# Optimization experiments

Hardware: AMD Instinct MI355X
Metric: run time of the kernel (lower is better)

Reference implementation:

```python
import jax, jax.numpy as jnp
import numpy as np


def _matrix_sqrt(x, iter_n=3):
    # Newton-Schulz iteration for batched matrix square root. x: [B, d, d]
    norm = jnp.linalg.norm(x, axis=(1, 2), keepdims=True)
    Y = x / (norm + 1e-8)
    d = x.shape[1]
    I = jnp.broadcast_to(jnp.eye(d, dtype=x.dtype), x.shape)
    Z = I
    for _ in range(iter_n):
        T = 0.5 * (3.0 * I - Z @ Y)
        Y = Y @ T
        Z = T @ Z
    return Y * jnp.sqrt(norm + 1e-8)


def _l2norm(x, eps=1e-12):
    n = jnp.linalg.norm(x, axis=-1, keepdims=True)
    return x / jnp.maximum(n, eps)


def _tukey(x, beta=0.5):
    return jnp.sign(x) * jnp.power(jnp.abs(x) + 1e-8, beta)


def _components(feat, cov_reducer, w_bls, b_bls):
    # feat: [Bx, N, D] patch tokens for one layer
    gap = feat.mean(axis=1)                                   # [Bx, D]
    x = feat @ cov_reducer                                    # [Bx, N, P]
    x = x - x.mean(axis=1, keepdims=True)
    denom = max(1, feat.shape[1] - 1)
    cov = jnp.einsum('bnp,bnq->bpq', x, x) / denom            # [Bx, P, P]
    P = cov.shape[-1]
    cov = cov + 1e-5 * jnp.eye(P, dtype=cov.dtype)
    cs = _matrix_sqrt(cov)
    iu = np.triu_indices(P)
    cov_flat = cs[:, iu[0], iu[1]]                            # [Bx, P*(P+1)/2]
    bls = jnp.tanh(feat @ w_bls + b_bls).mean(axis=1)         # [Bx, W]
    return gap, cov_flat, bls


def _fuse(gap, cov, bls, n_views):
    # gap/cov/bls: [L, Bx, F_l]; concat layers, pool views, tukey + l2 + weight
    def proc(t, w):
        Bx = t.shape[1]
        t = jnp.moveaxis(t, 0, 1).reshape(Bx, -1)             # cat over layers
        t = t.reshape(-1, n_views, t.shape[-1]).mean(axis=1)  # TTA view pooling
        return _l2norm(_tukey(t)) * w
    return jnp.concatenate([proc(gap, 1.0), proc(cov, 0.8), proc(bls, 0.1)], axis=-1)


def _forward(feats_sup, feats_qry, cov_reducer, w_bls, b_bls, y_sup, B, n_views, num_classes):
    comp = jax.vmap(_components, in_axes=(0, None, None, None))
    gs, cs, bs = comp(feats_sup, cov_reducer, w_bls, b_bls)
    gq, cq, bq = comp(feats_qry, cov_reducer, w_bls, b_bls)
    z_sup = _fuse(gs, cs, bs, n_views)
    z_qry = _fuse(gq, cq, bq, n_views)
    z_sup = z_sup.reshape(B, -1, z_sup.shape[-1])             # [B, n_sup, d]
    z_qry = z_qry.reshape(B, -1, z_qry.shape[-1])             # [B, n_qry, d]
    mu_sup = z_sup.mean(axis=1, keepdims=True)
    std_sup = jnp.std(z_sup, axis=1, keepdims=True, ddof=1) + 1e-8
    mu_qry = z_qry.mean(axis=1, keepdims=True)
    std_qry = jnp.std(z_qry, axis=1, keepdims=True, ddof=1) + 1e-8
    z_qry = (z_qry - mu_qry) / std_qry * std_sup + mu_sup
    z_sup = _l2norm(z_sup - mu_sup)
    z_qry = _l2norm(z_qry - mu_sup)
    Y = jax.nn.one_hot(y_sup, num_classes, dtype=z_sup.dtype)
    d_feat = z_sup.shape[-1]
    lam = 0.1 * (d_feat / 500.0)
    n_sup = z_sup.shape[1]
    K = jnp.einsum('bnd,bmd->bnm', z_sup, z_sup)
    alpha = jnp.linalg.solve(K + lam * jnp.eye(n_sup, dtype=K.dtype), Y)
    sim = jnp.einsum('bqd,bnd->bqn', z_qry, z_sup)
    return (sim @ alpha) * 20.0


def setup_inputs() -> dict:
    key = jax.random.key(0)
    ks = jax.random.split(key, 5)
    L, N, D, P = 2, 196, 768, 64
    B, n_sup, n_qry, n_views = 2, 25, 50, 5
    feats_sup = jax.random.normal(ks[0], (L, B * n_sup * n_views, N, D), jnp.float32)
    feats_qry = jax.random.normal(ks[1], (L, B * n_qry * n_views, N, D), jnp.float32)
    y_sup = jax.random.randint(ks[2], (B, n_sup), 0, 5)
    cov_reducer = jax.random.normal(ks[3], (D, P), jnp.float32) / jnp.sqrt(jnp.float32(D))
    w_bls = jax.random.normal(ks[4], (D, D), jnp.float32) / jnp.sqrt(jnp.float32(D))
    b_bls = jnp.zeros((D,), jnp.float32)
    return {"feats_sup": feats_sup, "feats_qry": feats_qry, "cov_reducer": cov_reducer,
            "w_bls": w_bls, "b_bls": b_bls, "y_sup": y_sup, "B": B, "n_views": n_views,
            "num_classes": 5}


def reference(feats_sup, feats_qry, cov_reducer, w_bls, b_bls, y_sup, B, n_views, num_classes):
    return _forward(feats_sup, feats_qry, cov_reducer, w_bls, b_bls, y_sup, B, n_views, num_classes)
```

## Files before the change

### kernel.cpp

```cpp
#include <hip/hip_runtime.h>
#include <stdint.h>
#include <math.h>

typedef __bf16 bf16x8_t __attribute__((ext_vector_type(8)));
typedef float  f32x4_t  __attribute__((ext_vector_type(4)));

constexpr int NTOK = 196;
constexpr int DF   = 768;
constexpr int PD   = 64;
constexpr int NSAMP = 1500;
constexpr int SUPS  = 500;
constexpr int PFLAT = 2080;
constexpr int FTOT  = 7232;
constexpr size_t FEAT_ELEMS = (size_t)NTOK * DF;

constexpr size_t SZ_FEATB = (size_t)NSAMP * FEAT_ELEMS * 2;
constexpr size_t OFF_FEATB = 0;
constexpr size_t OFF_WT    = OFF_FEATB + SZ_FEATB;
constexpr size_t SZ_WT     = (size_t)DF * DF * 2;
constexpr size_t OFF_RTH   = OFF_WT + SZ_WT;
constexpr size_t SZ_RT     = (size_t)PD * DF * 2;
constexpr size_t OFF_RTL   = OFF_RTH + SZ_RT;
constexpr size_t OFF_GAP   = OFF_RTL + SZ_RT;
constexpr size_t SZ_GAP    = (size_t)NSAMP * DF * 4;
constexpr size_t OFF_BLS   = OFF_GAP + SZ_GAP;
constexpr size_t OFF_COVF  = OFF_BLS + SZ_GAP;
constexpr size_t SZ_COVF   = (size_t)NSAMP * PFLAT * 4;
constexpr size_t OFF_Z     = OFF_COVF + SZ_COVF;
constexpr size_t SZ_Z      = (size_t)150 * FTOT * 4;
constexpr size_t OFF_ZN    = OFF_Z + SZ_Z;
constexpr size_t OFF_STATS = OFF_ZN + SZ_Z;
constexpr size_t SZ_STATS  = (size_t)4 * 2 * FTOT * 4;
constexpr size_t OFF_KM    = OFF_STATS + SZ_STATS;
constexpr size_t OFF_SIM   = OFF_KM + 5120;

__device__ __forceinline__ unsigned short f2bf(float f) {
    unsigned int u = __float_as_uint(f);
    u += 0x7fffu + ((u >> 16) & 1u);
    return (unsigned short)(u >> 16);
}
__device__ __forceinline__ float bf2f(unsigned short h) {
    return __uint_as_float(((unsigned int)h) << 16);
}
__device__ __forceinline__ void async_copy16(void* lds, const void* g) {
    __builtin_amdgcn_global_load_lds(
        (const __attribute__((address_space(1))) unsigned int*)g,
        (__attribute__((address_space(3))) unsigned int*)lds, 16, 0, 0);
}
__device__ __forceinline__ f32x4_t mfma16(bf16x8_t a, bf16x8_t b, f32x4_t c) {
    return __builtin_amdgcn_mfma_f32_16x16x32_bf16(a, b, c, 0, 0, 0);
}
__device__ __forceinline__ float tukeyf(float x) {
    float s = (x > 0.f) ? 1.f : ((x < 0.f) ? -1.f : 0.f);
    return s * sqrtf(fabsf(x) + 1e-8f);
}
__device__ __forceinline__ float blockReduceSum(float v, float* scratch) {
    for (int m = 1; m < 64; m <<= 1) v += __shfl_xor(v, m);
    int w = threadIdx.x >> 6, lane = threadIdx.x & 63;
    if (lane == 0) scratch[w] = v;
    __syncthreads();
    float r = scratch[0] + scratch[1] + scratch[2] + scratch[3];
    __syncthreads();
    return r;
}

__global__ __launch_bounds__(256) void k_prep(const float* __restrict__ W,
                                              const float* __restrict__ red,
                                              unsigned short* __restrict__ Wt,
                                              unsigned short* __restrict__ rTh,
                                              unsigned short* __restrict__ rTl) {
    int tid = blockIdx.x * 256 + threadIdx.x;
    int stride = gridDim.x * 256;
    for (int idx = tid; idx < DF * DF; idx += stride) {
        int d = idx / DF, k = idx % DF;
        Wt[idx] = f2bf(W[k * DF + d]);
    }
    for (int idx = tid; idx < PD * DF; idx += stride) {
        int p = idx / DF, k = idx % DF;
        float v = red[k * PD + p];
        unsigned short h = f2bf(v);
        rTh[idx] = h;
        rTl[idx] = f2bf(v - bf2f(h));
    }
}

__global__ __launch_bounds__(256) void k_sample(const float* __restrict__ fsup,
                                                const float* __restrict__ fqry,
                                                const unsigned short* __restrict__ rTh,
                                                const unsigned short* __restrict__ rTl,
                                                unsigned short* __restrict__ featB,
                                                float* __restrict__ gapB,
                                                float* __restrict__ covF) {
    __shared__ __align__(16) char smem[67840];
    unsigned short* Ahi = (unsigned short*)smem;
    unsigned short* Alo = Ahi + 8192;
    unsigned short* Bhi = Alo + 8192;
    unsigned short* Blo = Bhi + 2048;
    float* xT    = (float*)smem;
    float* covB  = (float*)(smem + 50432);
    float* gscr  = (float*)(smem + 50432 + 16640);
    float* means = (float*)(smem + 50432 + 16640 + 512);

    int sid = blockIdx.x;
    const float* fbase = (sid < SUPS) ? (fsup + (size_t)sid * FEAT_ELEMS)
                                      : (fqry + (size_t)(sid - SUPS) * FEAT_ELEMS);
    unsigned short* fB = featB + (size_t)sid * FEAT_ELEMS;

    int t = threadIdx.x;
    int w = t >> 6, lane = t & 63;
    int kgroup = t & 7, rbase = t >> 3;

    f32x4_t acc[4][4];
    f32x4_t z4 = {0.f, 0.f, 0.f, 0.f};
    #pragma unroll
    for (int i = 0; i < 4; ++i)
        #pragma unroll
        for (int j = 0; j < 4; ++j) acc[i][j] = z4;

    for (int k0 = 0; k0 < DF; k0 += 32) {
        float gx = 0.f, gy = 0.f, gz = 0.f, gw = 0.f;
        #pragma unroll
        for (int it = 0; it < 8; ++it) {
            int row = rbase + 32 * it;
            int n = row < NTOK ? row : (NTOK - 1);
            float4 v = *(const float4*)(fbase + (size_t)n * DF + k0 + kgroup * 4);
            unsigned short h0 = f2bf(v.x), h1 = f2bf(v.y), h2 = f2bf(v.z), h3 = f2bf(v.w);
            ushort4 hv; hv.x = h0; hv.y = h1; hv.z = h2; hv.w = h3;
            ushort4 lv;
            lv.x = f2bf(v.x - bf2f(h0)); lv.y = f2bf(v.y - bf2f(h1));
            lv.z = f2bf(v.z - bf2f(h2)); lv.w = f2bf(v.w - bf2f(h3));
            *(ushort4*)(Ahi + row * 32 + kgroup * 4) = hv;
            *(ushort4*)(Alo + row * 32 + kgroup * 4) = lv;
            if (row < NTOK) {
                gx += v.x; gy += v.y; gz += v.z; gw += v.w;
                *(ushort4*)(fB + (size_t)row * DF + k0 + kgroup * 4) = hv;
            }
        }
        gx += __shfl_xor(gx, 8);  gy += __shfl_xor(gy, 8);  gz += __shfl_xor(gz, 8);  gw += __shfl_xor(gw, 8);
        gx += __shfl_xor(gx, 16); gy += __shfl_xor(gy, 16); gz += __shfl_xor(gz, 16); gw += __shfl_xor(gw, 16);
        gx += __shfl_xor(gx, 32); gy += __shfl_xor(gy, 32); gz += __shfl_xor(gz, 32); gw += __shfl_xor(gw, 32);
        if (lane < 8) {
            gscr[w * 32 + lane * 4 + 0] = gx; gscr[w * 32 + lane * 4 + 1] = gy;
            gscr[w * 32 + lane * 4 + 2] = gz; gscr[w * 32 + lane * 4 + 3] = gw;
        }
        {
            int p = t >> 2, kq = t & 3;
            *(bf16x8_t*)(Bhi + p * 32 + kq * 8) = *(const bf16x8_t*)(rTh + (size_t)p * DF + k0 + kq * 8);
            *(bf16x8_t*)(Blo + p * 32 + kq * 8) = *(const bf16x8_t*)(rTl + (size_t)p * DF + k0 + kq * 8);
        }
        __syncthreads();
        if (t < 32) {
            float s = gscr[t] + gscr[32 + t] + gscr[64 + t] + gscr[96 + t];
            gapB[(size_t)sid * DF + k0 + t] = s * (1.f / 196.f);
        }
        bf16x8_t ah[4], al[4], bh[4], bl[4];
        int krow = (lane >> 4) * 8;
        #pragma unroll
        for (int i = 0; i < 4; ++i) {
            int aoff = (w * 64 + i * 16 + (lane & 15)) * 32 + krow;
            ah[i] = *(const bf16x8_t*)&Ahi[aoff];
            al[i] = *(const bf16x8_t*)&Alo[aoff];
        }
        #pragma unroll
        for (int j = 0; j < 4; ++j) {
            int boff = (j * 16 + (lane & 15)) * 32 + krow;
            bh[j] = *(const bf16x8_t*)&Bhi[boff];
            bl[j] = *(const bf16x8_t*)&Blo[boff];
        }
        #pragma unroll
        for (int i = 0; i < 4; ++i)
            #pragma unroll
            for (int j = 0; j < 4; ++j) {
                acc[i][j] = mfma16(ah[i], bh[j], acc[i][j]);
                acc[i][j] = mfma16(ah[i], bl[j], acc[i][j]);
                acc[i][j] = mfma16(al[i], bh[j], acc[i][j]);
            }
        __syncthreads();
    }

    int quad = lane >> 4, col = lane & 15;
    #pragma unroll
    for (int i = 0; i < 4; ++i)
        #pragma unroll
        for (int j = 0; j < 4; ++j)
            #pragma unroll
            for (int r = 0; r < 4; ++r) {
                int rowN = w * 64 + i * 16 + quad * 4 + r;
                if (rowN < NTOK) xT[(j * 16 + col) * 197 + rowN] = acc[i][j][r];
            }
    __syncthreads();
    if (t < 64) {
        float s = 0.f;
        for (int n = 0; n < NTOK; ++n) s += xT[t * 197 + n];
        means[t] = s * (1.f / 196.f);
    }
    __syncthreads();
    {
        int p = t & 63;
        for (int n = t >> 6; n < NTOK; n += 4) xT[p * 197 + n] -= means[p];
    }
    __syncthreads();
    int tp = t >> 4, tq = t & 15;
    {
        float cc[4][4] = {{0.f}};
        for (int k = 0; k < NTOK; ++k) {
            float a_[4], b_[4];
            #pragma unroll
            for (int i = 0; i < 4; ++i) a_[i] = xT[(4 * tp + i) * 197 + k];
            #pragma unroll
            for (int j = 0; j < 4; ++j) b_[j] = xT[(4 * tq + j) * 197 + k];
            #pragma unroll
            for (int i = 0; i < 4; ++i)
                #pragma unroll
                for (int j = 0; j < 4; ++j) cc[i][j] += a_[i] * b_[j];
        }
        float ssq = 0.f;
        #pragma unroll
        for (int i = 0; i < 4; ++i)
            #pragma unroll
            for (int j = 0; j < 4; ++j) {
                int gi = 4 * tp + i, gj = 4 * tq + j;
                float cv = cc[i][j] * (1.f / 195.f);
                if (gi == gj) cv += 1e-5f;
                covB[gi * 65 + gj] = cv;
                ssq += cv * cv;
            }
        float tot = blockReduceSum(ssq, gscr);
        float norm = sqrtf(tot);
        float rn = 1.f / (norm + 1e-8f);
        float scs = sqrtf(norm + 1e-8f);
        float* Yp = xT;
        float* Zp = xT + 4160;
        float* Up = xT + 8320;
        float* Tp = covB;
        for (int e = 0; e < 16; ++e) {
            int idx = t + 256 * e;
            int i = idx >> 6, j = idx & 63;
            Yp[i * 65 + j] = covB[i * 65 + j] * rn;
            Zp[i * 65 + j] = (i == j) ? 1.f : 0.f;
        }
        __syncthreads();

        for (int itn = 0; itn < 3; ++itn) {
            {
                float dd[4][4] = {{0.f}};
                for (int k = 0; k < 64; ++k) {
                    float a_[4], b_[4];
                    #pragma unroll
                    for (int i = 0; i < 4; ++i) a_[i] = Zp[(4 * tp + i) * 65 + k];
                    #pragma unroll
                    for (int j = 0; j < 4; ++j) b_[j] = Yp[k * 65 + 4 * tq + j];
                    #pragma unroll
                    for (int i = 0; i < 4; ++i)
                        #pragma unroll
                        for (int j = 0; j < 4; ++j) dd[i][j] += a_[i] * b_[j];
                }
                #pragma unroll
                for (int i = 0; i < 4; ++i)
                    #pragma unroll
                    for (int j = 0; j < 4; ++j) {
                        int gi = 4 * tp + i, gj = 4 * tq + j;
                        Tp[gi * 65 + gj] = 0.5f * (((gi == gj) ? 3.f : 0.f) - dd[i][j]);
                    }
            }
            __syncthreads();
            {
                float dd[4][4] = {{0.f}};
                for (int k = 0; k < 64; ++k) {
                    float a_[4], b_[4];
                    #pragma unroll
                    for (int i = 0; i < 4; ++i) a_[i] = Yp[(4 * tp + i) * 65 + k];
                    #pragma unroll
                    for (int j = 0; j < 4; ++j) b_[j] = Tp[k * 65 + 4 * tq + j];
                    #pragma unroll
                    for (int i = 0; i < 4; ++i)
                        #pragma unroll
                        for (int j = 0; j < 4; ++j) dd[i][j] += a_[i] * b_[j];
                }
                #pragma unroll
                for (int i = 0; i < 4; ++i)
                    #pragma unroll
                    for (int j = 0; j < 4; ++j) Up[(4 * tp + i) * 65 + 4 * tq + j] = dd[i][j];
            }
            __syncthreads();
            {
                float dd[4][4] = {{0.f}};
                for (int k = 0; k < 64; ++k) {
                    float a_[4], b_[4];
                    #pragma unroll
                    for (int i = 0; i < 4; ++i) a_[i] = Tp[(4 * tp + i) * 65 + k];
                    #pragma unroll
                    for (int j = 0; j < 4; ++j) b_[j] = Zp[k * 65 + 4 * tq + j];
                    #pragma unroll
                    for (int i = 0; i < 4; ++i)
                        #pragma unroll
                        for (int j = 0; j < 4; ++j) dd[i][j] += a_[i] * b_[j];
                }
                #pragma unroll
                for (int i = 0; i < 4; ++i)
                    #pragma unroll
                    for (int j = 0; j < 4; ++j) Yp[(4 * tp + i) * 65 + 4 * tq + j] = dd[i][j];
            }
            __syncthreads();
            float* ny = Up; float* nz = Yp; float* nu = Zp;
            Yp = ny; Zp = nz; Up = nu;
        }
        for (int idx = t; idx < PFLAT; idx += 256) {
            float disc = 129.f * 129.f - 8.f * (float)idx;
            int i = (int)((129.f - sqrtf(disc)) * 0.5f);
            if (i > 63) i = 63; if (i < 0) i = 0;
            while (i < 63 && ((i + 1) * 64 - ((i + 1) * i) / 2) <= idx) ++i;
            while (i > 0 && (i * 64 - (i * (i - 1)) / 2) > idx) --i;
            int S = i * 64 - (i * (i - 1)) / 2;
            int j = idx - S + i;
            covF[(size_t)sid * PFLAT + idx] = Yp[i * 65 + j] * scs;
        }
    }
}

__global__ __launch_bounds__(256) void k_bls(const unsigned short* __restrict__ featB,
                                             const unsigned short* __restrict__ Wt,
                                             const float* __restrict__ b_bls,
                                             float* __restrict__ blsB) {
    __shared__ unsigned short Al[128 * 32];
    __shared__ unsigned short Bl[128 * 32];
    __shared__ float colsum[128];

    int blk = blockIdx.x;
    int sid = blk / 6, dt = blk % 6;
    int d0 = dt * 128;
    size_t sidElems = (size_t)sid * FEAT_ELEMS;

    int t = threadIdx.x;
    int w = t >> 6, lane = t & 63;
    int wm = w >> 1, wn = w & 1;
    if (t < 128) colsum[t] = 0.f;

    for (int mt = 0; mt < 2; ++mt) {
        int m0 = mt * 128;
        f32x4_t acc[4][4];
        f32x4_t z4 = {0.f, 0.f, 0.f, 0.f};
        #pragma unroll
        for (int i = 0; i < 4; ++i)
            #pragma unroll
            for (int j = 0; j < 4; ++j) acc[i][j] = z4;

        for (int k0 = 0; k0 < DF; k0 += 32) {
            #pragma unroll
            for (int jj = 0; jj < 2; ++jj) {
                int j = 2 * w + jj;
                int row = j * 16 + (lane >> 2);
                int chunk = lane & 3;
                int gr = m0 + row; gr = gr > 195 ? 195 : gr;
                async_copy16((char*)Al + j * 1024 + lane * 16,
                             featB + sidElems + (size_t)gr * DF + k0 + chunk * 8);
                async_copy16((char*)Bl + j * 1024 + lane * 16,
                             Wt + (size_t)(d0 + row) * DF + k0 + chunk * 8);
            }
            __syncthreads();

            bf16x8_t af[4], bfr[4];
            int krow = (lane >> 4) * 8;
            #pragma unroll
            for (int i = 0; i < 4; ++i)
                af[i] = *(const bf16x8_t*)&Al[(wm * 64 + i * 16 + (lane & 15)) * 32 + krow];
            #pragma unroll
            for (int j = 0; j < 4; ++j)
                bfr[j] = *(const bf16x8_t*)&Bl[(wn * 64 + j * 16 + (lane & 15)) * 32 + krow];
            #pragma unroll
            for (int i = 0; i < 4; ++i)
                #pragma unroll
                for (int j = 0; j < 4; ++j)
                    acc[i][j] = mfma16(af[i], bfr[j], acc[i][j]);
            __syncthreads();
        }
        int quad = lane >> 4, col = lane & 15;
        #pragma unroll
        for (int j = 0; j < 4; ++j) {
            int dl = wn * 64 + j * 16 + col;
            float bb = b_bls[d0 + dl];
            float psum = 0.f;
            #pragma unroll
            for (int i = 0; i < 4; ++i)
                #pragma unroll
                for (int r = 0; r < 4; ++r) {
                    int rowN = m0 + wm * 64 + i * 16 + quad * 4 + r;
                    if (rowN < NTOK) psum += tanhf(acc[i][j][r] + bb);
                }
            psum += __shfl_xor(psum, 16);
            psum += __shfl_xor(psum, 32);
            if (quad == 0) atomicAdd(&colsum[dl], psum);
        }
    }
    __syncthreads();
    if (t < 128) blsB[(size_t)sid * DF + d0 + t] = colsum[t] * (1.f / 196.f);
}

__global__ __launch_bounds__(256) void k_fuse(const float* __restrict__ gapB,
                                              const float* __restrict__ covF,
                                              const float* __restrict__ blsB,
                                              float* __restrict__ z) {
    __shared__ float zrow[FTOT];
    __shared__ float scr[8];
    int r = blockIdx.x, t = threadIdx.x;
    bool isSup = r < 50;
    int g = isSup ? r : r - 50;

    float ss0 = 0.f, ss1 = 0.f, ss2 = 0.f;
    for (int f = t; f < DF; f += 256) {
        for (int l = 0; l < 2; ++l) {
            float s = 0.f;
            for (int v = 0; v < 5; ++v) {
                int sid = isSup ? (l * 250 + g * 5 + v) : (500 + l * 500 + g * 5 + v);
                s += gapB[(size_t)sid * DF + f];
            }
            float tk = tukeyf(s * 0.2f);
            zrow[l * DF + f] = tk;
            ss0 += tk * tk;
        }
    }
    for (int f = t; f < PFLAT; f += 256) {
        for (int l = 0; l < 2; ++l) {
            float s = 0.f;
            for (int v = 0; v < 5; ++v) {
                int sid = isSup ? (l * 250 + g * 5 + v) : (500 + l * 500 + g * 5 + v);
                s += covF[(size_t)sid * PFLAT + f];
            }
            float tk = tukeyf(s * 0.2f);
            zrow[1536 + l * PFLAT + f] = tk;
            ss1 += tk * tk;
        }
    }
    for (int f = t; f < DF; f += 256) {
        for (int l = 0; l < 2; ++l) {
            float s = 0.f;
            for (int v = 0; v < 5; ++v) {
                int sid = isSup ? (l * 250 + g * 5 + v) : (500 + l * 500 + g * 5 + v);
                s += blsB[(size_t)sid * DF + f];
            }
            float tk = tukeyf(s * 0.2f);
            zrow[5696 + l * DF + f] = tk;
            ss2 += tk * tk;
        }
    }
    __syncthreads();
    float n0 = blockReduceSum(ss0, scr);
    float n1 = blockReduceSum(ss1, scr);
    float n2 = blockReduceSum(ss2, scr);
    float s0 = 1.0f / fmaxf(sqrtf(n0), 1e-12f);
    float s1 = 0.8f / fmaxf(sqrtf(n1), 1e-12f);
    float s2 = 0.1f / fmaxf(sqrtf(n2), 1e-12f);
    for (int f = t; f < FTOT; f += 256) {
        float sc = (f < 1536) ? s0 : ((f < 5696) ? s1 : s2);
        z[(size_t)r * FTOT + f] = zrow[f] * sc;
    }
}

__global__ __launch_bounds__(256) void k_stats(const float* __restrict__ z,
                                               float* __restrict__ stats) {
    int f = blockIdx.x * 256 + threadIdx.x;
    int b = blockIdx.y;
    if (f >= FTOT) return;
    float mu = 0.f;
    for (int i = 0; i < 25; ++i) mu += z[(size_t)(b * 25 + i) * FTOT + f];
    mu *= (1.f / 25.f);
    float var = 0.f;
    for (int i = 0; i < 25; ++i) { float d = z[(size_t)(b * 25 + i) * FTOT + f] - mu; var += d * d; }
    float sds = sqrtf(var * (1.f / 24.f)) + 1e-8f;
    float muq = 0.f;
    for (int q = 0; q < 50; ++q) muq += z[(size_t)(50 + b * 50 + q) * FTOT + f];
    muq *= (1.f / 50.f);
    float varq = 0.f;
    for (int q = 0; q < 50; ++q) { float d = z[(size_t)(50 + b * 50 + q) * FTOT + f] - muq; varq += d * d; }
    float sdq = sqrtf(varq * (1.f / 49.f)) + 1e-8f;
    stats[(0 * 2 + b) * FTOT + f] = mu;
    stats[(1 * 2 + b) * FTOT + f] = sds;
    stats[(2 * 2 + b) * FTOT + f] = muq;
    stats[(3 * 2 + b) * FTOT + f] = sdq;
}

__global__ __launch_bounds__(256) void k_norm2(const float* __restrict__ z,
                                               const float* __restrict__ stats,
                                               float* __restrict__ zn) {
    __shared__ float scr[8];
    int r = blockIdx.x, t = threadIdx.x;
    bool isSup = r < 50;
    int b = isSup ? (r / 25) : ((r - 50) / 50);
    const float* mu_s = stats + (size_t)(0 * 2 + b) * FTOT;
    const float* sd_s = stats + (size_t)(1 * 2 + b) * FTOT;
    const float* mu_q = stats + (size_t)(2 * 2 + b) * FTOT;
    const float* sd_q = stats + (size_t)(3 * 2 + b) * FTOT;
    float ssq = 0.f;
    for (int f = t; f < FTOT; f += 256) {
        float v;
        float zv = z[(size_t)r * FTOT + f];
        if (isSup) v = zv - mu_s[f];
        else {
            float q = (zv - mu_q[f]) / sd_q[f] * sd_s[f] + mu_s[f];
            v = q - mu_s[f];
        }
        zn[(size_t)r * FTOT + f] = v;
        ssq += v * v;
    }
    float tot = blockReduceSum(ssq, scr);
    float sc = 1.f / fmaxf(sqrtf(tot), 1e-12f);
    for (int f = t; f < FTOT; f += 256) zn[(size_t)r * FTOT + f] *= sc;
}

__global__ __launch_bounds__(256) void k_gram(const float* __restrict__ zn,
                                              float* __restrict__ Km,
                                              float* __restrict__ simB) {
    __shared__ float scr[8];
    int r = blockIdx.x, t = threadIdx.x;
    bool isSup = r < 50;
    int b = isSup ? (r / 25) : ((r - 50) / 50);
    const float* a = zn + (size_t)r * FTOT;
    for (int j = 0; j < 25; ++j) {
        const float* bj = zn + (size_t)(b * 25 + j) * FTOT;
        float p = 0.f;
        for (int f = t; f < FTOT; f += 256) p += a[f] * bj[f];
        float tot = blockReduceSum(p, scr);
        if (t == 0) {
            if (isSup) Km[b * 625 + (r - b * 25) * 25 + j] = tot;
            else       simB[b * 1250 + (r - 50 - b * 50) * 25 + j] = tot;
        }
    }
}

__global__ __launch_bounds__(256) void k_solve(const float* __restrict__ Km,
                                               const float* __restrict__ simB,
                                               const int* __restrict__ y_sup,
                                               float* __restrict__ out) {
    __shared__ float A[25][31];
    __shared__ float alpha[25][5];
    int b = blockIdx.x, t = threadIdx.x;
    const float lam = 0.1f * (7232.0f / 500.0f);
    for (int idx = t; idx < 625; idx += 256) {
        int i = idx / 25, j = idx % 25;
        A[i][j] = Km[b * 625 + idx] + ((i == j) ? lam : 0.f);
    }
    for (int idx = t; idx < 125; idx += 256) {
        int i = idx / 5, c = idx % 5;
        A[i][25 + c] = (y_sup[b * 25 + i] == c) ? 1.f : 0.f;
    }
    __syncthreads();
    for (int k = 0; k < 25; ++k) {
        if (t > k && t < 25) {
            float f = A[t][k] / A[k][k];
            for (int c = k; c < 30; ++c) A[t][c] -= f * A[k][c];
        }
        __syncthreads();
    }
    for (int k = 24; k >= 0; --k) {
        if (t < 5) {
            float s = A[k][25 + t];
            for (int j = k + 1; j < 25; ++j) s -= A[k][j] * alpha[j][t];
            alpha[k][t] = s / A[k][k];
        }
        __syncthreads();
    }
    for (int idx = t; idx < 250; idx += 256) {
        int q = idx / 5, c = idx % 5;
        float s = 0.f;
        for (int n = 0; n < 25; ++n) s += simB[b * 1250 + q * 25 + n] * alpha[n][c];
        out[(b * 50 + q) * 5 + c] = 20.f * s;
    }
}

extern "C" void kernel_launch(void* const* d_in, const int* in_sizes, int n_in,
                              void* d_out, int out_size, void* d_ws, size_t ws_size,
                              hipStream_t stream) {
    const float* fsup  = (const float*)d_in[0];
    const float* fqry  = (const float*)d_in[1];
    const float* red   = (const float*)d_in[2];
    const float* Wb    = (const float*)d_in[3];
    const float* b_bls = (const float*)d_in[4];
    const int*   y_sup = (const int*)d_in[5];
    float* out = (float*)d_out;
    char* ws = (char*)d_ws;

    unsigned short* featB = (unsigned short*)(ws + OFF_FEATB);
    unsigned short* Wt    = (unsigned short*)(ws + OFF_WT);
    unsigned short* rTh   = (unsigned short*)(ws + OFF_RTH);
    unsigned short* rTl   = (unsigned short*)(ws + OFF_RTL);
    float* gapB  = (float*)(ws + OFF_GAP);
    float* blsB  = (float*)(ws + OFF_BLS);
    float* covF  = (float*)(ws + OFF_COVF);
    float* z     = (float*)(ws + OFF_Z);
    float* zn    = (float*)(ws + OFF_ZN);
    float* stats = (float*)(ws + OFF_STATS);
    float* Km    = (float*)(ws + OFF_KM);
    float* simB  = (float*)(ws + OFF_SIM);

    k_prep<<<dim3(512), dim3(256), 0, stream>>>(Wb, red, Wt, rTh, rTl);
    k_sample<<<dim3(NSAMP), dim3(256), 0, stream>>>(fsup, fqry, rTh, rTl, featB, gapB, covF);
    k_bls<<<dim3(NSAMP * 6), dim3(256), 0, stream>>>(featB, Wt, b_bls, blsB);
    k_fuse<<<dim3(150), dim3(256), 0, stream>>>(gapB, covF, blsB, z);
    k_stats<<<dim3((FTOT + 255) / 256, 2), dim3(256), 0, stream>>>(z, stats);
    k_norm2<<<dim3(150), dim3(256), 0, stream>>>(z, stats, zn);
    k_gram<<<dim3(150), dim3(256), 0, stream>>>(zn, Km, simB);
    k_solve<<<dim3(2), dim3(256), 0, stream>>>(Km, simB, y_sup, out);
}
```

Before: 2.670 ms.

## Flatten BLS GEMM across samples with double-buffered swizzled LDS and fast tanh

The BLS GEMM now treats all samples' tokens as one flat M dimension, so tiles no longer waste rows padding each sample's 196 tokens up to 256. Column sums are written with global atomics split across at most two samples per tile, and the output is zeroed in the prep kernel. The kernel also double-buffers LDS staging with an XOR swizzle, remaps blocks across XCDs, and uses an exp/rcp tanh approximation. The approximation adds some floating-point error, and atomics make summation order nondeterministic.

```diff
diff --git a/kernel.cpp b/kernel.cpp
--- a/kernel.cpp
+++ b/kernel.cpp
@@ -13,6 +13,9 @@
 constexpr int PFLAT = 2080;
 constexpr int FTOT  = 7232;
 constexpr size_t FEAT_ELEMS = (size_t)NTOK * DF;
+constexpr int MROWS  = NSAMP * NTOK;
+constexpr int MTILES = (MROWS + 127) / 128;
+constexpr int BLS_WGS = MTILES * 6;
 
 constexpr size_t SZ_FEATB = (size_t)NSAMP * FEAT_ELEMS * 2;
 constexpr size_t OFF_FEATB = 0;
@@ -54,6 +57,10 @@
     float s = (x > 0.f) ? 1.f : ((x < 0.f) ? -1.f : 0.f);
     return s * sqrtf(fabsf(x) + 1e-8f);
 }
+__device__ __forceinline__ float fast_tanh(float x) {
+    float e = __expf(2.f * x);
+    return 1.f - 2.f * __builtin_amdgcn_rcpf(e + 1.f);
+}
 __device__ __forceinline__ float blockReduceSum(float v, float* scratch) {
     for (int m = 1; m < 64; m <<= 1) v += __shfl_xor(v, m);
     int w = threadIdx.x >> 6, lane = threadIdx.x & 63;
@@ -68,7 +75,8 @@
                                               const float* __restrict__ red,
                                               unsigned short* __restrict__ Wt,
                                               unsigned short* __restrict__ rTh,
-                                              unsigned short* __restrict__ rTl) {
+                                              unsigned short* __restrict__ rTl,
+                                              float* __restrict__ blsB) {
     int tid = blockIdx.x * 256 + threadIdx.x;
     int stride = gridDim.x * 256;
     for (int idx = tid; idx < DF * DF; idx += stride) {
@@ -82,6 +90,7 @@
         rTh[idx] = h;
         rTl[idx] = f2bf(v - bf2f(h));
     }
+    for (int idx = tid; idx < NSAMP * DF; idx += stride) blsB[idx] = 0.f;
 }
 
 __global__ __launch_bounds__(256) void k_sample(const float* __restrict__ fsup,
@@ -318,82 +327,99 @@
     }
 }
 
-__global__ __launch_bounds__(256) void k_bls(const unsigned short* __restrict__ featB,
-                                             const unsigned short* __restrict__ Wt,
-                                             const float* __restrict__ b_bls,
-                                             float* __restrict__ blsB) {
-    __shared__ unsigned short Al[128 * 32];
-    __shared__ unsigned short Bl[128 * 32];
-    __shared__ float colsum[128];
-
-    int blk = blockIdx.x;
-    int sid = blk / 6, dt = blk % 6;
+__global__ __launch_bounds__(256, 4) void k_bls(const unsigned short* __restrict__ featB,
+                                                const unsigned short* __restrict__ Wt,
+                                                const float* __restrict__ b_bls,
+                                                float* __restrict__ blsB) {
+    __shared__ __align__(16) unsigned short Al[2][128 * 32];
+    __shared__ __align__(16) unsigned short Bl[2][128 * 32];
+
+    constexpr int nwg = BLS_WGS;
+    constexpr int q = nwg >> 3, rr = nwg & 7;
+    int xcd = blockIdx.x & 7, bidx = blockIdx.x >> 3;
+    int logical = (xcd < rr ? xcd * (q + 1) : rr * (q + 1) + (xcd - rr) * q) + bidx;
+    int mtile = logical / 6, dt = logical % 6;
+    int R0 = mtile * 128;
     int d0 = dt * 128;
-    size_t sidElems = (size_t)sid * FEAT_ELEMS;
 
     int t = threadIdx.x;
     int w = t >> 6, lane = t & 63;
     int wm = w >> 1, wn = w & 1;
-    if (t < 128) colsum[t] = 0.f;
-
-    for (int mt = 0; mt < 2; ++mt) {
-        int m0 = mt * 128;
-        f32x4_t acc[4][4];
-        f32x4_t z4 = {0.f, 0.f, 0.f, 0.f};
+    int col = lane & 15, g = lane >> 4, quad = lane >> 4;
+
+    f32x4_t acc[4][4];
+    f32x4_t z4 = {0.f, 0.f, 0.f, 0.f};
+    #pragma unroll
+    for (int i = 0; i < 4; ++i)
+        #pragma unroll
+        for (int j = 0; j < 4; ++j) acc[i][j] = z4;
+
+    auto stage = [&](int buf, int k0) {
+        #pragma unroll
+        for (int l = 0; l < 2; ++l) {
+            int cid = l * 256 + t;
+            int r = cid >> 2;
+            int cg = (cid & 3) ^ ((r >> 1) & 3);
+            int Rg = R0 + r; if (Rg >= MROWS) Rg = MROWS - 1;
+            async_copy16((char*)&Al[buf][0] + (size_t)cid * 16,
+                         featB + (size_t)Rg * DF + k0 + cg * 8);
+            async_copy16((char*)&Bl[buf][0] + (size_t)cid * 16,
+                         Wt + (size_t)(d0 + r) * DF + k0 + cg * 8);
+        }
+    };
+
+    stage(0, 0);
+    asm volatile("s_waitcnt vmcnt(0)" ::: "memory");
+    __builtin_amdgcn_s_barrier();
+
+    int swc = (g ^ ((col >> 1) & 3)) * 8;
+    int cur = 0;
+    for (int ks = 0; ks < DF / 32; ++ks) {
+        if (ks + 1 < DF / 32) stage(cur ^ 1, (ks + 1) * 32);
+        bf16x8_t af[4], bfr[4];
         #pragma unroll
         for (int i = 0; i < 4; ++i)
-            #pragma unroll
-            for (int j = 0; j < 4; ++j) acc[i][j] = z4;
-
-        for (int k0 = 0; k0 < DF; k0 += 32) {
-            #pragma unroll
-            for (int jj = 0; jj < 2; ++jj) {
-                int j = 2 * w + jj;
-                int row = j * 16 + (lane >> 2);
-                int chunk = lane & 3;
-                int gr = m0 + row; gr = gr > 195 ? 195 : gr;
-                async_copy16((char*)Al + j * 1024 + lane * 16,
-                             featB + sidElems + (size_t)gr * DF + k0 + chunk * 8);
-                async_copy16((char*)Bl + j * 1024 + lane * 16,
-                             Wt + (size_t)(d0 + row) * DF + k0 + chunk * 8);
-            }
-            __syncthreads();
-
-            bf16x8_t af[4], bfr[4];
-            int krow = (lane >> 4) * 8;
-            #pragma unroll
-            for (int i = 0; i < 4; ++i)
-                af[i] = *(const bf16x8_t*)&Al[(wm * 64 + i * 16 + (lane & 15)) * 32 + krow];
+            af[i] = *(const bf16x8_t*)&Al[cur][(wm * 64 + i * 16 + col) * 32 + swc];
+        #pragma unroll
+        for (int j = 0; j < 4; ++j)
+            bfr[j] = *(const bf16x8_t*)&Bl[cur][(wn * 64 + j * 16 + col) * 32 + swc];
+        #pragma unroll
+        for (int i = 0; i < 4; ++i)
             #pragma unroll
             for (int j = 0; j < 4; ++j)
-                bfr[j] = *(const bf16x8_t*)&Bl[(wn * 64 + j * 16 + (lane & 15)) * 32 + krow];
-            #pragma unroll
-            for (int i = 0; i < 4; ++i)
-                #pragma unroll
-                for (int j = 0; j < 4; ++j)
-                    acc[i][j] = mfma16(af[i], bfr[j], acc[i][j]);
-            __syncthreads();
-        }
-        int quad = lane >> 4, col = lane & 15;
-        #pragma unroll
-        for (int j = 0; j < 4; ++j) {
-            int dl = wn * 64 + j * 16 + col;
-            float bb = b_bls[d0 + dl];
-            float psum = 0.f;
-            #pragma unroll
-            for (int i = 0; i < 4; ++i)
-                #pragma unroll
-                for (int r = 0; r < 4; ++r) {
-                    int rowN = m0 + wm * 64 + i * 16 + quad * 4 + r;
-                    if (rowN < NTOK) psum += tanhf(acc[i][j][r] + bb);
+                acc[i][j] = mfma16(af[i], bfr[j], acc[i][j]);
+        if (ks + 1 < DF / 32) {
+            asm volatile("s_waitcnt vmcnt(0)" ::: "memory");
+            __builtin_amdgcn_s_barrier();
+            cur ^= 1;
+        }
+    }
+
+    int sid0 = R0 / NTOK;
+    int bnd = sid0 * NTOK + NTOK;
+    #pragma unroll
+    for (int j = 0; j < 4; ++j) {
+        int d = d0 + wn * 64 + j * 16 + col;
+        float bb = b_bls[d];
+        float p0 = 0.f, p1 = 0.f;
+        #pragma unroll
+        for (int i = 0; i < 4; ++i)
+            #pragma unroll
+            for (int r = 0; r < 4; ++r) {
+                int Rg = R0 + wm * 64 + i * 16 + quad * 4 + r;
+                if (Rg < MROWS) {
+                    float v = fast_tanh(acc[i][j][r] + bb);
+                    if (Rg < bnd) p0 += v; else p1 += v;
                 }
-            psum += __shfl_xor(psum, 16);
-            psum += __shfl_xor(psum, 32);
-            if (quad == 0) atomicAdd(&colsum[dl], psum);
-        }
-    }
-    __syncthreads();
-    if (t < 128) blsB[(size_t)sid * DF + d0 + t] = colsum[t] * (1.f / 196.f);
+            }
+        p0 += __shfl_xor(p0, 16); p0 += __shfl_xor(p0, 32);
+        p1 += __shfl_xor(p1, 16); p1 += __shfl_xor(p1, 32);
+        if (quad == 0) {
+            if (p0 != 0.f) atomicAdd(&blsB[(size_t)sid0 * DF + d], p0 * (1.f / 196.f));
+            if (p1 != 0.f && sid0 + 1 < NSAMP)
+                atomicAdd(&blsB[(size_t)(sid0 + 1) * DF + d], p1 * (1.f / 196.f));
+        }
+    }
 }
 
 __global__ __launch_bounds__(256) void k_fuse(const float* __restrict__ gapB,
@@ -592,9 +618,9 @@
     float* Km    = (float*)(ws + OFF_KM);
     float* simB  = (float*)(ws + OFF_SIM);
 
-    k_prep<<<dim3(512), dim3(256), 0, stream>>>(Wb, red, Wt, rTh, rTl);
+    k_prep<<<dim3(512), dim3(256), 0, stream>>>(Wb, red, Wt, rTh, rTl, blsB);
     k_sample<<<dim3(NSAMP), dim3(256), 0, stream>>>(fsup, fqry, rTh, rTl, featB, gapB, covF);
-    k_bls<<<dim3(NSAMP * 6), dim3(256), 0, stream>>>(featB, Wt, b_bls, blsB);
+    k_bls<<<dim3(BLS_WGS), dim3(256), 0, stream>>>(featB, Wt, b_bls, blsB);
     k_fuse<<<dim3(150), dim3(256), 0, stream>>>(gapB, covF, blsB, z);
     k_stats<<<dim3((FTOT + 255) / 256, 2), dim3(256), 0, stream>>>(z, stats);
     k_norm2<<<dim3(150), dim3(256), 0, stream>>>(z, stats, zn);
```

New measurement: 2.201 ms. 17.6% less time.
